# Kernel tuning notes

Measured on AMD Instinct MI355X. Metric: run time of the kernel, lower is better.

The kernel has to match this reference:

```python
import jax, jax.numpy as jnp
import numpy as np
from jax import lax

# --- Clifford algebra Cl(3,0): sig_g = [1,1,1], n_blades = 8 ---
SIG = np.array([1.0, 1.0, 1.0], dtype=np.float32)
N_GEN = len(SIG)
N_BLADES = 1 << N_GEN

def _build_cayley(g):
    # Structure constants C[a,b,c]: e_a * e_b = C[a,b,a^b] * e_{a^b}
    n = len(g); nb = 1 << n
    C = np.zeros((nb, nb, nb), dtype=np.float32)
    for a in range(nb):
        for b in range(nb):
            s = 1.0
            x = a >> 1
            while x:
                if bin(x & b).count('1') % 2:
                    s = -s
                x >>= 1
            common = a & b
            for k in range(n):
                if (common >> k) & 1:
                    s *= g[k]
            C[a, b, a ^ b] = s
    return C

CAYLEY = _build_cayley(SIG)
# blade signs: scalar coefficient of e_i * e_i (metric square of each blade)
BLADE_SIGNS = np.array([CAYLEY[i, i, 0] for i in range(N_BLADES)], dtype=np.float32)

DT = 0.1      # EPEngine dt
N_FREE = 5    # EPEngine n_free

def _energy(h, input_mv, W_rec, C, signs):
    # h: [B,L,H,I]
    rho = jnp.clip(h, 0.0, 1.0)
    E_self = 0.5 * jnp.sum(h * h, axis=(1, 2, 3))                       # [B]
    E_in = jnp.einsum('blhi,blhi,i->b', rho, input_mv, signs)           # [B]
    # causal recurrent term: geometric product of h_{l-1} with W_rec
    rec = jnp.einsum('blhi,ghj,ijk->blgk', rho[:, :-1], W_rec, C)       # [B,L-1,H,I]
    E_rec = jnp.einsum('blhk,blhk,k->b', rho[:, 1:], rec, signs)        # [B]
    return E_self - E_in - E_rec

def _free_phase(h0, input_mv, W_rec, C, signs):
    gfn = jax.grad(lambda h: jnp.sum(_energy(h, input_mv, W_rec, C, signs)))
    def step(h, _):
        return h - DT * gfn(h), None
    h, _ = lax.scan(step, h0, None, length=N_FREE)
    return h

def setup_inputs() -> dict:
    key = jax.random.key(0)
    ks = jax.random.split(key, 5)
    B, L, V, E, H = 4, 256, 32000, 256, 256
    x = jax.random.randint(ks[0], (B, L), 0, V)
    emb_table = jax.random.normal(ks[1], (V, E), jnp.float32)
    W_in = jax.random.normal(ks[2], (H, E, N_BLADES), jnp.float32) * 0.1
    W_rec = jax.random.normal(ks[3], (H, H, N_BLADES), jnp.float32) * 0.05
    W_out = jax.random.normal(ks[4], (V, H, N_BLADES), jnp.float32) * 0.1
    return {"x": x, "emb_table": emb_table, "W_in": W_in, "W_rec": W_rec, "W_out": W_out}

def reference(x, emb_table, W_in, W_rec, W_out):
    C = jnp.asarray(CAYLEY)
    signs = jnp.asarray(BLADE_SIGNS)
    emb = emb_table[x]                                  # [B,L,E]
    input_mv = jnp.einsum('bld,hdi->blhi', emb, W_in)   # [B,L,H,I]
    B, L = x.shape
    H = W_in.shape[0]
    h0 = jnp.zeros((B, L, H, N_BLADES), jnp.float32)
    h_free = _free_phase(h0, input_mv, W_rec, C, signs) # [B,L,H,I]
    # scalar part of geometric product of h_free with W_out (only blade 0 kept)
    logits = jnp.einsum('blhi,vhj,ij->blv', h_free, W_out, C[:, :, 0])
    return logits
```

## Files before the change

kernel.cpp:

```cpp
#include <hip/hip_runtime.h>
#include <cstddef>
#include <cstdint>

#define VOCAB  32000
#define EMB    256
#define NB     8
#define KDIM   2048
#define NROWS  1024
#define NCOL   4096
#define LLEN   256

typedef __attribute__((ext_vector_type(8))) short short8;
typedef __attribute__((ext_vector_type(4))) float f32x4;
typedef __attribute__((ext_vector_type(16))) float f32x16;
typedef __attribute__((ext_vector_type(4))) int i32x4;
typedef __attribute__((ext_vector_type(16))) int i32x16;

__device__ __forceinline__ float cl3_sign(int a, int b) {
  int x = a >> 1, p = 0;
  while (x) { p ^= __popc(x & b) & 1; x >>= 1; }
  return p ? -1.f : 1.f;
}

__device__ __forceinline__ float clipf(float v) { return fminf(fmaxf(v, 0.f), 1.f); }

__device__ __forceinline__ unsigned short f2bf(float f) {
  unsigned u = __float_as_uint(f);
  u += 0x7FFF + ((u >> 16) & 1);
  return (unsigned short)(u >> 16);
}
__device__ __forceinline__ float bf2f(unsigned short h) {
  return __uint_as_float(((unsigned)h) << 16);
}

__device__ __forceinline__ void gload16(const void* g, void* l) {
  __builtin_amdgcn_global_load_lds((const __attribute__((address_space(1))) uint32_t*)g,
                                   (__attribute__((address_space(3))) uint32_t*)l, 16, 0, 0);
}

__device__ __forceinline__ float dig_inv(float mx) {
  return exp2f((float)(5 - ilogbf(fmaxf(mx, 1e-20f))));
}

__device__ __forceinline__ size_t bfoff(int rt, int k, int r) {
  return ((size_t)(rt * 128 + (k >> 4)) << 11) + (size_t)(((k >> 3) & 1) << 10) + ((r & 127) << 3) + (k & 7);
}

__global__ void k_build_mrt_split(const float* __restrict__ Wrec,
                                  unsigned short* __restrict__ Mhi,
                                  unsigned short* __restrict__ Mlo) {
  int idx = blockIdx.x * blockDim.x + threadIdx.x;
  int k = idx & (KDIM - 1);
  int n = idx >> 11;
  int h = k >> 3, i = k & 7;
  float v;
  if (n < KDIM) {
    int g = n >> 3, kb = n & 7;
    int j = i ^ kb;
    v = Wrec[(size_t)g * KDIM + h * NB + j] * cl3_sign(i, j);
  } else {
    int c = n - KDIM;
    int p = c >> 3, q = c & 7;
    int j = q ^ i;
    v = cl3_sign(i, i) * cl3_sign(q, j) * Wrec[(size_t)h * KDIM + p * NB + j];
  }
  unsigned short hi = f2bf(v);
  unsigned short lo = f2bf(v - bf2f(hi));
  size_t off = bfoff(n >> 7, k, n);
  Mhi[off] = hi; Mlo[off] = lo;
}

__global__ __launch_bounds__(256) void k_dig_wout(const float* __restrict__ W,
                                                  float* __restrict__ sB,
                                                  char* __restrict__ Wd1,
                                                  char* __restrict__ Wd2) {
  __shared__ float ld[4 * 2052];
  __shared__ float rmax[4];
  const int t = threadIdx.x;
  const int bid = blockIdx.x;
  const float* src = W + (size_t)bid * 8192;
#pragma unroll
  for (int i = 0; i < 8; ++i) {
    int f = i * 256 + t;
    int row = f >> 9, c4 = f & 511;
    float4 v = ((const float4*)src)[f];
    *(float4*)&ld[row * 2052 + c4 * 4] = v;
  }
  __syncthreads();
  const int w = t >> 6, l = t & 63;
  float m = 0.f;
#pragma unroll
  for (int j = 0; j < 8; ++j) {
    float4 v = *(const float4*)&ld[w * 2052 + (j * 64 + l) * 4];
    m = fmaxf(m, fmaxf(fmaxf(fabsf(v.x), fabsf(v.y)), fmaxf(fabsf(v.z), fabsf(v.w))));
  }
#pragma unroll
  for (int s = 1; s < 64; s <<= 1) m = fmaxf(m, __shfl_xor(m, s));
  m = fmaxf(m, 1e-20f);
  if (l == 0) { rmax[w] = m; sB[bid * 4 + w] = exp2f((float)(ilogbf(m) + 2)); }
  __syncthreads();
  const int rloc = t & 3;
  const int rowg = bid * 4 + rloc;
  const int rowtile = rowg >> 7, rowin = rowg & 127;
  const float inv = dig_inv(rmax[rloc]);
#pragma unroll
  for (int it = 0; it < 2; ++it) {
    int c16 = (t >> 2) + it * 64;
    char d1[16], d2[16];
#pragma unroll
    for (int j = 0; j < 16; ++j) {
      float tv = ld[rloc * 2052 + c16 * 16 + j] * inv;
      float f1 = rintf(tv);
      d1[j] = (char)(int)f1;
      d2[j] = (char)(int)rintf((tv - f1) * 128.f);
    }
    size_t addr = ((size_t)(rowtile * 64 + (c16 >> 1)) << 12) + (size_t)((c16 & 1) << 11) + (rowin << 4);
    *(i32x4*)&Wd1[addr] = *(i32x4*)d1;
    *(i32x4*)&Wd2[addr] = *(i32x4*)d2;
  }
}

__global__ __launch_bounds__(256) void k_input_mv(const int* __restrict__ x,
                                                  const float* __restrict__ emb,
                                                  const float* __restrict__ Win,
                                                  float* __restrict__ out) {
  __shared__ float se[4][EMB];
  int r0 = blockIdx.x * 4;
  int t = threadIdx.x;
  for (int rr = 0; rr < 4; ++rr) {
    int tok = x[r0 + rr];
    se[rr][t] = emb[(size_t)tok * EMB + t];
  }
  __syncthreads();
  float acc[4][8];
#pragma unroll
  for (int rr = 0; rr < 4; ++rr)
#pragma unroll
    for (int i = 0; i < 8; ++i) acc[rr][i] = 0.f;
  const float* wrow = Win + (size_t)t * KDIM;
  for (int d = 0; d < EMB; ++d) {
    float4 w0 = *(const float4*)(wrow + d * 8);
    float4 w1 = *(const float4*)(wrow + d * 8 + 4);
#pragma unroll
    for (int rr = 0; rr < 4; ++rr) {
      float e = se[rr][d];
      acc[rr][0] += e * w0.x; acc[rr][1] += e * w0.y;
      acc[rr][2] += e * w0.z; acc[rr][3] += e * w0.w;
      acc[rr][4] += e * w1.x; acc[rr][5] += e * w1.y;
      acc[rr][6] += e * w1.z; acc[rr][7] += e * w1.w;
    }
  }
  for (int rr = 0; rr < 4; ++rr) {
    float4* o = (float4*)(out + (size_t)(r0 + rr) * KDIM + t * 8);
    o[0] = make_float4(acc[rr][0], acc[rr][1], acc[rr][2], acc[rr][3]);
    o[1] = make_float4(acc[rr][4], acc[rr][5], acc[rr][6], acc[rr][7]);
  }
}

__global__ __launch_bounds__(256, 2) void k_gemm_pre(const unsigned short* __restrict__ Ahi,
                                                     const unsigned short* __restrict__ Alo,
                                                     const unsigned short* __restrict__ Bhi,
                                                     const unsigned short* __restrict__ Blo,
                                                     float* __restrict__ RF0,
                                                     float* __restrict__ RF1) {
  __shared__ __align__(16) char lds[3 * 16384];
  const int b = blockIdx.x;
  const int lin = (b & 7) * 64 + (b >> 3);
  const int half = lin >> 8;
  const int rest = lin & 255;
  const int tm = rest & 7, tn = rest >> 3;
  const int ktbase = half * 64;
  float* __restrict__ C = half ? RF1 : RF0;
  const int t = threadIdx.x;
  const int l = t & 63, w = t >> 6;
  const int wr = w >> 1, wc = w & 1;

  const char* aHg = (const char*)Ahi + (((size_t)tm * 128 + ktbase) << 12) + (t << 4);
  const char* aLg = (const char*)Alo + (((size_t)tm * 128 + ktbase) << 12) + (t << 4);
  const char* bHg = (const char*)Bhi + (((size_t)tn * 128 + ktbase) << 12) + (t << 4);
  const char* bLg = (const char*)Blo + (((size_t)tn * 128 + ktbase) << 12) + (t << 4);
  const int wo = w << 10;

  f32x16 acc[2][2];
#pragma unroll
  for (int i = 0; i < 2; ++i)
#pragma unroll
    for (int j = 0; j < 2; ++j) acc[i][j] = (f32x16)0.f;

  auto STAGE = [&](int bf, int kt) {
    char* lb = &lds[bf * 16384];
    size_t kb = (size_t)kt << 12;
    gload16(aHg + kb, lb + wo);
    gload16(aLg + kb, lb + 4096 + wo);
    gload16(bHg + kb, lb + 8192 + wo);
    gload16(bLg + kb, lb + 12288 + wo);
  };

  STAGE(0, 0); STAGE(1, 1);

  const int ra = wr * 64 + (l & 31);
  const int rb = wc * 64 + (l & 31);
  const int cho = (l >> 5) << 11;
  int cur = 0;
  for (int kt = 0; kt < 64; ++kt) {
    int pf = cur + 2; if (pf >= 3) pf -= 3;
    if (kt < 63) { asm volatile("s_waitcnt vmcnt(4)" ::: "memory"); }
    else         { asm volatile("s_waitcnt vmcnt(0)" ::: "memory"); }
    __builtin_amdgcn_s_barrier();
    const char* lb = &lds[cur * 16384];
    short8 ah[2], al[2], bh[2], bl[2];
#pragma unroll
    for (int mi = 0; mi < 2; ++mi) {
      int off = cho + ((ra + mi * 32) << 4);
      ah[mi] = *(const short8*)(lb + off);
      al[mi] = *(const short8*)(lb + 4096 + off);
    }
#pragma unroll
    for (int nj = 0; nj < 2; ++nj) {
      int off = cho + ((rb + nj * 32) << 4);
      bh[nj] = *(const short8*)(lb + 8192 + off);
      bl[nj] = *(const short8*)(lb + 12288 + off);
    }
    if (kt + 2 < 64) STAGE(pf, kt + 2);
    __builtin_amdgcn_s_setprio(1);
#pragma unroll
    for (int mi = 0; mi < 2; ++mi)
#pragma unroll
      for (int nj = 0; nj < 2; ++nj) {
        acc[mi][nj] = __builtin_amdgcn_mfma_f32_32x32x16_bf16(ah[mi], bh[nj], acc[mi][nj], 0, 0, 0);
        acc[mi][nj] = __builtin_amdgcn_mfma_f32_32x32x16_bf16(ah[mi], bl[nj], acc[mi][nj], 0, 0, 0);
        acc[mi][nj] = __builtin_amdgcn_mfma_f32_32x32x16_bf16(al[mi], bh[nj], acc[mi][nj], 0, 0, 0);
      }
    __builtin_amdgcn_s_setprio(0);
    cur = (cur == 2) ? 0 : cur + 1;
  }

  const int rg0 = tm * 128 + wr * 64 + ((l >> 5) << 2);
  const int cg0 = tn * 128 + wc * 64 + (l & 31);
#pragma unroll
  for (int mi = 0; mi < 2; ++mi)
#pragma unroll
    for (int nj = 0; nj < 2; ++nj) {
      f32x16 v = acc[mi][nj];
#pragma unroll
      for (int g = 0; g < 16; ++g) {
        int rr = (g & 3) + ((g >> 2) << 3);
        C[(size_t)(rg0 + mi * 32 + rr) * NCOL + cg0 + nj * 32] = v[g];
      }
    }
}

__global__ __launch_bounds__(256, 2) void k_gemm_i8(const char* __restrict__ Ad1,
                                                    const char* __restrict__ Ad2,
                                                    const char* __restrict__ Bd1,
                                                    const char* __restrict__ Bd2,
                                                    const float* __restrict__ sA,
                                                    const float* __restrict__ sB,
                                                    float* __restrict__ C) {
  __shared__ __align__(16) char lds[3 * 16384];
  const int b = blockIdx.x;
  const int lin = (b & 7) * 250 + (b >> 3);
  const int tm = lin & 7, tn = lin >> 3;
  const int t = threadIdx.x;
  const int l = t & 63, w = t >> 6;
  const int wr = w >> 1, wc = w & 1;

  const char* a1g = Ad1 + (((size_t)tm * 64) << 12) + (t << 4);
  const char* a2g = Ad2 + (((size_t)tm * 64) << 12) + (t << 4);
  const char* b1g = Bd1 + (((size_t)tn * 64) << 12) + (t << 4);
  const char* b2g = Bd2 + (((size_t)tn * 64) << 12) + (t << 4);
  const int wo = w << 10;

  i32x16 acc1[2][2], acc2[2][2];
#pragma unroll
  for (int i = 0; i < 2; ++i)
#pragma unroll
    for (int j = 0; j < 2; ++j) { acc1[i][j] = (i32x16)0; acc2[i][j] = (i32x16)0; }

  auto STAGE = [&](int bf, int kt) {
    char* lb = &lds[bf * 16384];
    size_t kb = (size_t)kt << 12;
    gload16(a1g + kb, lb + wo);
    gload16(a2g + kb, lb + 4096 + wo);
    gload16(b1g + kb, lb + 8192 + wo);
    gload16(b2g + kb, lb + 12288 + wo);
  };

  STAGE(0, 0); STAGE(1, 1);

  const int ra = wr * 64 + (l & 31);
  const int rb = wc * 64 + (l & 31);
  const int kqo = (l >> 5) << 11;
  int cur = 0;
  for (int kt = 0; kt < 64; ++kt) {
    int pf = cur + 2; if (pf >= 3) pf -= 3;
    if (kt < 63) { asm volatile("s_waitcnt vmcnt(4)" ::: "memory"); }
    else         { asm volatile("s_waitcnt vmcnt(0)" ::: "memory"); }
    __builtin_amdgcn_s_barrier();
    const char* lb = &lds[cur * 16384];
    i32x4 a1[2], a2[2], b1[2], b2[2];
#pragma unroll
    for (int mi = 0; mi < 2; ++mi) {
      int off = kqo + ((ra + mi * 32) << 4);
      a1[mi] = *(const i32x4*)(lb + off);
      a2[mi] = *(const i32x4*)(lb + 4096 + off);
    }
#pragma unroll
    for (int nj = 0; nj < 2; ++nj) {
      int off = kqo + ((rb + nj * 32) << 4);
      b1[nj] = *(const i32x4*)(lb + 8192 + off);
      b2[nj] = *(const i32x4*)(lb + 12288 + off);
    }
    if (kt + 2 < 64) STAGE(pf, kt + 2);
    __builtin_amdgcn_s_setprio(1);
#pragma unroll
    for (int mi = 0; mi < 2; ++mi)
#pragma unroll
      for (int nj = 0; nj < 2; ++nj) {
        acc1[mi][nj] = __builtin_amdgcn_mfma_i32_32x32x32_i8(a1[mi], b1[nj], acc1[mi][nj], 0, 0, 0);
        acc2[mi][nj] = __builtin_amdgcn_mfma_i32_32x32x32_i8(a1[mi], b2[nj], acc2[mi][nj], 0, 0, 0);
        acc2[mi][nj] = __builtin_amdgcn_mfma_i32_32x32x32_i8(a2[mi], b1[nj], acc2[mi][nj], 0, 0, 0);
      }
    __builtin_amdgcn_s_setprio(0);
    cur = (cur == 2) ? 0 : cur + 1;
  }

  const int rbase = tm * 128 + wr * 64 + ((l >> 5) << 2);
  const int cb = tn * 128 + wc * 64 + (l & 31);
#pragma unroll
  for (int mi = 0; mi < 2; ++mi)
#pragma unroll
    for (int nj = 0; nj < 2; ++nj) {
      float sBv = sB[cb + nj * 32] * (1.f / 16384.f);
#pragma unroll
      for (int g = 0; g < 16; ++g) {
        int rr = (g & 3) + ((g >> 2) << 3);
        int row = rbase + mi * 32 + rr;
        float c1 = sA[row] * sBv;
        C[(size_t)row * VOCAB + cb + nj * 32] =
            fmaf((float)acc2[mi][nj][g], c1 * (1.f / 128.f), (float)acc1[mi][nj][g] * c1);
      }
    }
}

template <int LAST, int FIRST>
__global__ __launch_bounds__(256) void k_update(float* __restrict__ Hb, const float* __restrict__ Imv,
                                                const float* __restrict__ RF0, const float* __restrict__ RF1,
                                                unsigned short* __restrict__ Hhi,
                                                unsigned short* __restrict__ Hlo,
                                                float* __restrict__ sA,
                                                char* __restrict__ Ad1,
                                                char* __restrict__ Ad2,
                                                int big) {
  __shared__ float red[256];
  int tix = threadIdx.x;
  int idx = blockIdx.x * 256 + tix;
  int r = idx >> 8;
  int c = (idx & 255) << 3;
  int m = r & (LLEN - 1);
  const size_t base = (size_t)r * KDIM + c;
  float h[8], f[8];
  *(float4*)&h[0] = *(const float4*)(Hb + base);
  *(float4*)&h[4] = *(const float4*)(Hb + base + 4);
  float4 i0 = *(const float4*)(Imv + base);
  float4 i1 = *(const float4*)(Imv + base + 4);
  f[0] = i0.x; f[1] = i0.y; f[2] = i0.z; f[3] = i0.w;
  f[4] = i1.x; f[5] = i1.y; f[6] = i1.z; f[7] = i1.w;
#pragma unroll
  for (int j = 0; j < 8; ++j) f[j] *= ((0xE8 >> j) & 1) ? -1.f : 1.f;
  if (!FIRST) {
    if (m >= 1) {
      const float* rp0 = RF0 + (size_t)(r - 1) * NCOL + c;
      const float* rp1 = RF1 + (size_t)(r - 1) * NCOL + c;
#pragma unroll
      for (int j = 0; j < 8; ++j)
        f[j] += (rp0[j] + rp1[j]) * (((0xE8 >> j) & 1) ? -1.f : 1.f);
    }
    if (m < LLEN - 1) {
      const float* rn0 = RF0 + (size_t)(r + 1) * NCOL + KDIM + c;
      const float* rn1 = RF1 + (size_t)(r + 1) * NCOL + KDIM + c;
#pragma unroll
      for (int j = 0; j < 8; ++j) f[j] += rn0[j] + rn1[j];
    }
  }
  float hn[8], av[8];
#pragma unroll
  for (int j = 0; j < 8; ++j) {
    float hv = h[j];
    float dr = (hv > 0.f && hv < 1.f) ? 1.f : ((hv == 0.f || hv == 1.f) ? 0.5f : 0.f);
    hn[j] = hv - 0.1f * (hv - dr * f[j]);
  }
  *(float4*)(Hb + base) = make_float4(hn[0], hn[1], hn[2], hn[3]);
  *(float4*)(Hb + base + 4) = make_float4(hn[4], hn[5], hn[6], hn[7]);
  if (!LAST) {
    short8 h8, l8;
#pragma unroll
    for (int j = 0; j < 8; ++j) {
      float a = clipf(hn[j]);
      unsigned short hi = f2bf(a);
      h8[j] = (short)hi;
      l8[j] = (short)f2bf(a - bf2f(hi));
    }
    size_t off = bfoff(r >> 7, c, r);
    *(short8*)&Hhi[off] = h8;
    *(short8*)&Hlo[off] = l8;
  } else {
    if (!big) return;
#pragma unroll
    for (int j = 0; j < 8; ++j) av[j] = hn[j] * (((0xE8 >> j) & 1) ? -1.f : 1.f);
    float lm = 0.f;
#pragma unroll
    for (int j = 0; j < 8; ++j) lm = fmaxf(lm, fabsf(av[j]));
    red[tix] = lm; __syncthreads();
    for (int s = 128; s; s >>= 1) { if (tix < s) red[tix] = fmaxf(red[tix], red[tix + s]); __syncthreads(); }
    float mx = fmaxf(red[0], 1e-20f);
    float inv = dig_inv(mx);
    if (tix == 0) sA[r] = exp2f((float)(ilogbf(mx) + 2));
    char d1[8], d2[8];
#pragma unroll
    for (int j = 0; j < 8; ++j) {
      float tv = av[j] * inv;
      float f1 = rintf(tv);
      d1[j] = (char)(int)f1;
      d2[j] = (char)(int)rintf((tv - f1) * 128.f);
    }
    size_t addr = ((size_t)((r >> 7) * 64 + (c >> 5)) << 12) + (size_t)(((c >> 4) & 1) << 11)
                + ((r & 127) << 4) + (c & 15);
    *(uint64_t*)&Ad1[addr] = *(uint64_t*)d1;
    *(uint64_t*)&Ad2[addr] = *(uint64_t*)d2;
  }
}

template <int AMODE>
__global__ __launch_bounds__(256) void k_gemm_split(const float* __restrict__ A,
                                                    const float* __restrict__ B,
                                                    float* __restrict__ C, int ldc) {
  __shared__ unsigned short Ah[128 * 32], Al[128 * 32];
  __shared__ unsigned short Bh[128 * 32], Bl[128 * 32];
  const int t = threadIdx.x;
  const int row0 = blockIdx.y * 128, col0 = blockIdx.x * 128;
  const int l = t & 63, w = t >> 6;
  const int wr = w >> 1, wc = w & 1;
  const int sr = t >> 3;
  const int cc = (t & 7) << 2;
  const int chunkb = cc >> 3;
  const int halfo = (cc >> 2) & 1;
  f32x4 acc[4][4];
#pragma unroll
  for (int i = 0; i < 4; ++i)
#pragma unroll
    for (int j = 0; j < 4; ++j) acc[i][j] = (f32x4)0.f;
  const float sA0 = 1.f;
  const float sA1 = (cc & 4) ? -1.f : 1.f;
  const float sA2 = sA1;
  const float sA3 = -1.f;
  for (int k0 = 0; k0 < KDIM; k0 += 32) {
    float4 va[4], vb[4];
#pragma unroll
    for (int i = 0; i < 4; ++i) {
      va[i] = *(const float4*)(A + (size_t)(row0 + sr + i * 32) * KDIM + k0 + cc);
      vb[i] = *(const float4*)(B + (size_t)(col0 + sr + i * 32) * KDIM + k0 + cc);
    }
    __syncthreads();
#pragma unroll
    for (int i = 0; i < 4; ++i) {
      int row = sr + i * 32;
      int idx = row * 32 + ((chunkb ^ (row & 3)) << 3) + (halfo << 2);
      float4 a = va[i];
      if (AMODE == 0) {
        a.x = clipf(a.x); a.y = clipf(a.y); a.z = clipf(a.z); a.w = clipf(a.w);
      } else {
        a.x *= sA0; a.y *= sA1; a.z *= sA2; a.w *= sA3;
      }
      ushort4 h4, l4;
      h4.x = f2bf(a.x); l4.x = f2bf(a.x - bf2f(h4.x));
      h4.y = f2bf(a.y); l4.y = f2bf(a.y - bf2f(h4.y));
      h4.z = f2bf(a.z); l4.z = f2bf(a.z - bf2f(h4.z));
      h4.w = f2bf(a.w); l4.w = f2bf(a.w - bf2f(h4.w));
      *(ushort4*)&Ah[idx] = h4;
      *(ushort4*)&Al[idx] = l4;
      float4 bb = vb[i];
      h4.x = f2bf(bb.x); l4.x = f2bf(bb.x - bf2f(h4.x));
      h4.y = f2bf(bb.y); l4.y = f2bf(bb.y - bf2f(h4.y));
      h4.z = f2bf(bb.z); l4.z = f2bf(bb.z - bf2f(h4.z));
      h4.w = f2bf(bb.w); l4.w = f2bf(bb.w - bf2f(h4.w));
      *(ushort4*)&Bh[idx] = h4;
      *(ushort4*)&Bl[idx] = l4;
    }
    __syncthreads();
    short8 ah[4], al[4], bh[4], bl[4];
#pragma unroll
    for (int mi = 0; mi < 4; ++mi) {
      int ar = wr * 64 + mi * 16 + (l & 15);
      int kc = (l >> 4) ^ (ar & 3);
      ah[mi] = *(short8*)&Ah[ar * 32 + kc * 8];
      al[mi] = *(short8*)&Al[ar * 32 + kc * 8];
      int br = wc * 64 + mi * 16 + (l & 15);
      int kb = (l >> 4) ^ (br & 3);
      bh[mi] = *(short8*)&Bh[br * 32 + kb * 8];
      bl[mi] = *(short8*)&Bl[br * 32 + kb * 8];
    }
#pragma unroll
    for (int mi = 0; mi < 4; ++mi)
#pragma unroll
      for (int ni = 0; ni < 4; ++ni) {
        acc[mi][ni] = __builtin_amdgcn_mfma_f32_16x16x32_bf16(ah[mi], bh[ni], acc[mi][ni], 0, 0, 0);
        acc[mi][ni] = __builtin_amdgcn_mfma_f32_16x16x32_bf16(ah[mi], bl[ni], acc[mi][ni], 0, 0, 0);
        acc[mi][ni] = __builtin_amdgcn_mfma_f32_16x16x32_bf16(al[mi], bh[ni], acc[mi][ni], 0, 0, 0);
      }
  }
#pragma unroll
  for (int mi = 0; mi < 4; ++mi)
#pragma unroll
    for (int ni = 0; ni < 4; ++ni) {
      int rg = row0 + wr * 64 + mi * 16 + (l >> 4) * 4;
      int cg = col0 + wc * 64 + ni * 16 + (l & 15);
#pragma unroll
      for (int j = 0; j < 4; ++j)
        C[(size_t)(rg + j) * ldc + cg] = acc[mi][ni][j];
    }
}

extern "C" void kernel_launch(void* const* d_in, const int* in_sizes, int n_in,
                              void* d_out, int out_size, void* d_ws, size_t ws_size,
                              hipStream_t stream) {
  const int*   x    = (const int*)d_in[0];
  const float* emb  = (const float*)d_in[1];
  const float* Win  = (const float*)d_in[2];
  const float* Wrec = (const float*)d_in[3];
  const float* Wout = (const float*)d_in[4];
  float* logits = (float*)d_out;

  char* base = (char*)d_ws;
  const size_t MB = 1ull << 20;
  float* Hbuf = (float*)(base + 0);
  float* Imv  = (float*)(base + 8 * MB);
  float* RF0  = (float*)(base + 16 * MB);
  float* RF1  = (float*)(base + 32 * MB);
  unsigned short* Hhi = (unsigned short*)(base + 48 * MB);
  unsigned short* Hlo = (unsigned short*)(base + 52 * MB);
  unsigned short* Mhi = (unsigned short*)(base + 56 * MB);
  unsigned short* Mlo = (unsigned short*)(base + 72 * MB);
  float* sA  = (float*)(base + 88 * MB);
  float* sB  = (float*)(base + 88 * MB + 4096);
  char* Wd1  = base + 88 * MB + 160 * 1024;
  char* Wd2  = Wd1 + (size_t)VOCAB * KDIM;
  char* Ad1  = (char*)Mhi;
  char* Ad2  = (char*)Mlo;

  const size_t need = (size_t)(Wd2 - base) + (size_t)VOCAB * KDIM;
  const bool big = ws_size >= need;

  hipMemsetAsync(Hbuf, 0, 8 * MB, stream);
  k_build_mrt_split<<<32768, 256, 0, stream>>>(Wrec, Mhi, Mlo);
  k_input_mv<<<256, 256, 0, stream>>>(x, emb, Win, Imv);
  if (big) {
    k_dig_wout<<<8000, 256, 0, stream>>>(Wout, sB, Wd1, Wd2);
  }

  k_update<0, 1><<<1024, 256, 0, stream>>>(Hbuf, Imv, RF0, RF1, Hhi, Hlo, sA, Ad1, Ad2, big);
  for (int it = 1; it < 5; ++it) {
    k_gemm_pre<<<512, 256, 0, stream>>>(Hhi, Hlo, Mhi, Mlo, RF0, RF1);
    if (it < 4) k_update<0, 0><<<1024, 256, 0, stream>>>(Hbuf, Imv, RF0, RF1, Hhi, Hlo, sA, Ad1, Ad2, big);
    else        k_update<1, 0><<<1024, 256, 0, stream>>>(Hbuf, Imv, RF0, RF1, Hhi, Hlo, sA, Ad1, Ad2, big);
  }

  if (big) {
    k_gemm_i8<<<2000, 256, 0, stream>>>(Ad1, Ad2, Wd1, Wd2, sA, sB, logits);
  } else {
    k_gemm_split<1><<<dim3(VOCAB / 128, NROWS / 128), 256, 0, stream>>>(Hbuf, Wout, logits, VOCAB);
  }
}
```

Before: 631.2 us.

## Halve GEMM N-tile to 64 with higher occupancy and fuse first update into input_mv

```diff
diff --git a/kernel.cpp b/kernel.cpp
--- a/kernel.cpp
+++ b/kernel.cpp
@@ -120,10 +120,13 @@
   }
 }
 
-__global__ __launch_bounds__(256) void k_input_mv(const int* __restrict__ x,
+__global__ __launch_bounds__(256) void k_input_h1(const int* __restrict__ x,
                                                   const float* __restrict__ emb,
                                                   const float* __restrict__ Win,
-                                                  float* __restrict__ out) {
+                                                  float* __restrict__ Imv,
+                                                  float* __restrict__ Hb,
+                                                  unsigned short* __restrict__ Hhi,
+                                                  unsigned short* __restrict__ Hlo) {
   __shared__ float se[4][EMB];
   int r0 = blockIdx.x * 4;
   int t = threadIdx.x;
@@ -150,200 +153,208 @@
       acc[rr][6] += e * w1.z; acc[rr][7] += e * w1.w;
     }
   }
+  const int c = t * 8;
   for (int rr = 0; rr < 4; ++rr) {
-    float4* o = (float4*)(out + (size_t)(r0 + rr) * KDIM + t * 8);
-    o[0] = make_float4(acc[rr][0], acc[rr][1], acc[rr][2], acc[rr][3]);
-    o[1] = make_float4(acc[rr][4], acc[rr][5], acc[rr][6], acc[rr][7]);
-  }
-}
-
-__global__ __launch_bounds__(256, 2) void k_gemm_pre(const unsigned short* __restrict__ Ahi,
+    int r = r0 + rr;
+    float* o = Imv + (size_t)r * KDIM + c;
+    *(float4*)o = make_float4(acc[rr][0], acc[rr][1], acc[rr][2], acc[rr][3]);
+    *(float4*)(o + 4) = make_float4(acc[rr][4], acc[rr][5], acc[rr][6], acc[rr][7]);
+    float hn[8];
+    short8 h8, l8;
+#pragma unroll
+    for (int j = 0; j < 8; ++j) {
+      float f = acc[rr][j] * (((0xE8 >> j) & 1) ? -1.f : 1.f);
+      hn[j] = 0.f - 0.1f * (0.f - 0.5f * f);
+      float a = clipf(hn[j]);
+      unsigned short hi = f2bf(a);
+      h8[j] = (short)hi;
+      l8[j] = (short)f2bf(a - bf2f(hi));
+    }
+    float* hb = Hb + (size_t)r * KDIM + c;
+    *(float4*)hb = make_float4(hn[0], hn[1], hn[2], hn[3]);
+    *(float4*)(hb + 4) = make_float4(hn[4], hn[5], hn[6], hn[7]);
+    size_t off = bfoff(r >> 7, c, r);
+    *(short8*)&Hhi[off] = h8;
+    *(short8*)&Hlo[off] = l8;
+  }
+}
+
+__global__ __launch_bounds__(256, 4) void k_gemm_pre(const unsigned short* __restrict__ Ahi,
                                                      const unsigned short* __restrict__ Alo,
                                                      const unsigned short* __restrict__ Bhi,
                                                      const unsigned short* __restrict__ Blo,
                                                      float* __restrict__ RF0,
                                                      float* __restrict__ RF1) {
-  __shared__ __align__(16) char lds[3 * 16384];
+  __shared__ __align__(16) char lds[3 * 12288];
   const int b = blockIdx.x;
-  const int lin = (b & 7) * 64 + (b >> 3);
-  const int half = lin >> 8;
-  const int rest = lin & 255;
-  const int tm = rest & 7, tn = rest >> 3;
+  const int lin = (b & 7) * 128 + (b >> 3);
+  const int tm = lin & 7;
+  const int rest = lin >> 3;
+  const int tn = rest & 63, half = rest >> 6;
   const int ktbase = half * 64;
   float* __restrict__ C = half ? RF1 : RF0;
   const int t = threadIdx.x;
   const int l = t & 63, w = t >> 6;
   const int wr = w >> 1, wc = w & 1;
-
-  const char* aHg = (const char*)Ahi + (((size_t)tm * 128 + ktbase) << 12) + (t << 4);
-  const char* aLg = (const char*)Alo + (((size_t)tm * 128 + ktbase) << 12) + (t << 4);
-  const char* bHg = (const char*)Bhi + (((size_t)tn * 128 + ktbase) << 12) + (t << 4);
-  const char* bLg = (const char*)Blo + (((size_t)tn * 128 + ktbase) << 12) + (t << 4);
   const int wo = w << 10;
 
-  f32x16 acc[2][2];
-#pragma unroll
-  for (int i = 0; i < 2; ++i)
-#pragma unroll
-    for (int j = 0; j < 2; ++j) acc[i][j] = (f32x16)0.f;
+  const char* aHg = (const char*)Ahi + (((size_t)(tm * 128 + ktbase)) << 12) + (t << 4);
+  const char* aLg = (const char*)Alo + (((size_t)(tm * 128 + ktbase)) << 12) + (t << 4);
+  const int jj = t & 127;
+  const int bt = tn >> 1, r0b = (tn & 1) << 6;
+  const char* bGg = (const char*)((t >> 7) ? Blo : Bhi)
+                  + (((size_t)(bt * 128 + ktbase)) << 12)
+                  + ((jj >> 6) << 11) + ((size_t)(r0b + (jj & 63)) << 4);
+
+  f32x16 acc[2];
+  acc[0] = (f32x16)0.f; acc[1] = (f32x16)0.f;
 
   auto STAGE = [&](int bf, int kt) {
-    char* lb = &lds[bf * 16384];
+    char* lb = &lds[bf * 12288];
     size_t kb = (size_t)kt << 12;
     gload16(aHg + kb, lb + wo);
     gload16(aLg + kb, lb + 4096 + wo);
-    gload16(bHg + kb, lb + 8192 + wo);
-    gload16(bLg + kb, lb + 12288 + wo);
+    gload16(bGg + kb, lb + 8192 + wo);
   };
 
   STAGE(0, 0); STAGE(1, 1);
 
   const int ra = wr * 64 + (l & 31);
-  const int rb = wc * 64 + (l & 31);
-  const int cho = (l >> 5) << 11;
+  const int rb = wc * 32 + (l & 31);
+  const int kq = l >> 5;
   int cur = 0;
   for (int kt = 0; kt < 64; ++kt) {
     int pf = cur + 2; if (pf >= 3) pf -= 3;
-    if (kt < 63) { asm volatile("s_waitcnt vmcnt(4)" ::: "memory"); }
+    if (kt < 63) { asm volatile("s_waitcnt vmcnt(3)" ::: "memory"); }
     else         { asm volatile("s_waitcnt vmcnt(0)" ::: "memory"); }
     __builtin_amdgcn_s_barrier();
-    const char* lb = &lds[cur * 16384];
-    short8 ah[2], al[2], bh[2], bl[2];
+    const char* lb = &lds[cur * 12288];
+    short8 ah[2], al[2], bh, bl;
 #pragma unroll
     for (int mi = 0; mi < 2; ++mi) {
-      int off = cho + ((ra + mi * 32) << 4);
+      int off = (kq << 11) + ((ra + mi * 32) << 4);
       ah[mi] = *(const short8*)(lb + off);
       al[mi] = *(const short8*)(lb + 4096 + off);
     }
-#pragma unroll
-    for (int nj = 0; nj < 2; ++nj) {
-      int off = cho + ((rb + nj * 32) << 4);
-      bh[nj] = *(const short8*)(lb + 8192 + off);
-      bl[nj] = *(const short8*)(lb + 12288 + off);
+    {
+      int off = (kq << 10) + (rb << 4);
+      bh = *(const short8*)(lb + 8192 + off);
+      bl = *(const short8*)(lb + 10240 + off);
     }
     if (kt + 2 < 64) STAGE(pf, kt + 2);
     __builtin_amdgcn_s_setprio(1);
 #pragma unroll
-    for (int mi = 0; mi < 2; ++mi)
-#pragma unroll
-      for (int nj = 0; nj < 2; ++nj) {
-        acc[mi][nj] = __builtin_amdgcn_mfma_f32_32x32x16_bf16(ah[mi], bh[nj], acc[mi][nj], 0, 0, 0);
-        acc[mi][nj] = __builtin_amdgcn_mfma_f32_32x32x16_bf16(ah[mi], bl[nj], acc[mi][nj], 0, 0, 0);
-        acc[mi][nj] = __builtin_amdgcn_mfma_f32_32x32x16_bf16(al[mi], bh[nj], acc[mi][nj], 0, 0, 0);
-      }
+    for (int mi = 0; mi < 2; ++mi) {
+      acc[mi] = __builtin_amdgcn_mfma_f32_32x32x16_bf16(ah[mi], bh, acc[mi], 0, 0, 0);
+      acc[mi] = __builtin_amdgcn_mfma_f32_32x32x16_bf16(ah[mi], bl, acc[mi], 0, 0, 0);
+      acc[mi] = __builtin_amdgcn_mfma_f32_32x32x16_bf16(al[mi], bh, acc[mi], 0, 0, 0);
+    }
     __builtin_amdgcn_s_setprio(0);
     cur = (cur == 2) ? 0 : cur + 1;
   }
 
   const int rg0 = tm * 128 + wr * 64 + ((l >> 5) << 2);
-  const int cg0 = tn * 128 + wc * 64 + (l & 31);
-#pragma unroll
-  for (int mi = 0; mi < 2; ++mi)
-#pragma unroll
-    for (int nj = 0; nj < 2; ++nj) {
-      f32x16 v = acc[mi][nj];
-#pragma unroll
-      for (int g = 0; g < 16; ++g) {
-        int rr = (g & 3) + ((g >> 2) << 3);
-        C[(size_t)(rg0 + mi * 32 + rr) * NCOL + cg0 + nj * 32] = v[g];
-      }
-    }
-}
-
-__global__ __launch_bounds__(256, 2) void k_gemm_i8(const char* __restrict__ Ad1,
+  const int cg0 = tn * 64 + wc * 32 + (l & 31);
+#pragma unroll
+  for (int mi = 0; mi < 2; ++mi) {
+    f32x16 v = acc[mi];
+#pragma unroll
+    for (int g = 0; g < 16; ++g) {
+      int rr = (g & 3) + ((g >> 2) << 3);
+      C[(size_t)(rg0 + mi * 32 + rr) * NCOL + cg0] = v[g];
+    }
+  }
+}
+
+__global__ __launch_bounds__(256, 3) void k_gemm_i8(const char* __restrict__ Ad1,
                                                     const char* __restrict__ Ad2,
                                                     const char* __restrict__ Bd1,
                                                     const char* __restrict__ Bd2,
                                                     const float* __restrict__ sA,
                                                     const float* __restrict__ sB,
                                                     float* __restrict__ C) {
-  __shared__ __align__(16) char lds[3 * 16384];
+  __shared__ __align__(16) char lds[3 * 12288];
   const int b = blockIdx.x;
-  const int lin = (b & 7) * 250 + (b >> 3);
+  const int lin = (b & 7) * 500 + (b >> 3);
   const int tm = lin & 7, tn = lin >> 3;
   const int t = threadIdx.x;
   const int l = t & 63, w = t >> 6;
   const int wr = w >> 1, wc = w & 1;
+  const int wo = w << 10;
 
   const char* a1g = Ad1 + (((size_t)tm * 64) << 12) + (t << 4);
   const char* a2g = Ad2 + (((size_t)tm * 64) << 12) + (t << 4);
-  const char* b1g = Bd1 + (((size_t)tn * 64) << 12) + (t << 4);
-  const char* b2g = Bd2 + (((size_t)tn * 64) << 12) + (t << 4);
-  const int wo = w << 10;
-
-  i32x16 acc1[2][2], acc2[2][2];
-#pragma unroll
-  for (int i = 0; i < 2; ++i)
-#pragma unroll
-    for (int j = 0; j < 2; ++j) { acc1[i][j] = (i32x16)0; acc2[i][j] = (i32x16)0; }
+  const int jj = t & 127;
+  const int wt = tn >> 1, r0b = (tn & 1) << 6;
+  const char* bGg = ((t >> 7) ? Bd2 : Bd1)
+                  + (((size_t)wt * 64) << 12)
+                  + ((jj >> 6) << 11) + ((size_t)(r0b + (jj & 63)) << 4);
+
+  i32x16 acc1[2], acc2[2];
+  acc1[0] = (i32x16)0; acc1[1] = (i32x16)0;
+  acc2[0] = (i32x16)0; acc2[1] = (i32x16)0;
 
   auto STAGE = [&](int bf, int kt) {
-    char* lb = &lds[bf * 16384];
+    char* lb = &lds[bf * 12288];
     size_t kb = (size_t)kt << 12;
     gload16(a1g + kb, lb + wo);
     gload16(a2g + kb, lb + 4096 + wo);
-    gload16(b1g + kb, lb + 8192 + wo);
-    gload16(b2g + kb, lb + 12288 + wo);
+    gload16(bGg + kb, lb + 8192 + wo);
   };
 
   STAGE(0, 0); STAGE(1, 1);
 
   const int ra = wr * 64 + (l & 31);
-  const int rb = wc * 64 + (l & 31);
-  const int kqo = (l >> 5) << 11;
+  const int rb = wc * 32 + (l & 31);
+  const int kq = l >> 5;
   int cur = 0;
   for (int kt = 0; kt < 64; ++kt) {
     int pf = cur + 2; if (pf >= 3) pf -= 3;
-    if (kt < 63) { asm volatile("s_waitcnt vmcnt(4)" ::: "memory"); }
+    if (kt < 63) { asm volatile("s_waitcnt vmcnt(3)" ::: "memory"); }
     else         { asm volatile("s_waitcnt vmcnt(0)" ::: "memory"); }
     __builtin_amdgcn_s_barrier();
-    const char* lb = &lds[cur * 16384];
-    i32x4 a1[2], a2[2], b1[2], b2[2];
+    const char* lb = &lds[cur * 12288];
+    i32x4 a1[2], a2[2], b1, b2;
 #pragma unroll
     for (int mi = 0; mi < 2; ++mi) {
-      int off = kqo + ((ra + mi * 32) << 4);
+      int off = (kq << 11) + ((ra + mi * 32) << 4);
       a1[mi] = *(const i32x4*)(lb + off);
       a2[mi] = *(const i32x4*)(lb + 4096 + off);
     }
-#pragma unroll
-    for (int nj = 0; nj < 2; ++nj) {
-      int off = kqo + ((rb + nj * 32) << 4);
-      b1[nj] = *(const i32x4*)(lb + 8192 + off);
-      b2[nj] = *(const i32x4*)(lb + 12288 + off);
+    {
+      int off = (kq << 10) + (rb << 4);
+      b1 = *(const i32x4*)(lb + 8192 + off);
+      b2 = *(const i32x4*)(lb + 10240 + off);
     }
     if (kt + 2 < 64) STAGE(pf, kt + 2);
     __builtin_amdgcn_s_setprio(1);
 #pragma unroll
-    for (int mi = 0; mi < 2; ++mi)
-#pragma unroll
-      for (int nj = 0; nj < 2; ++nj) {
-        acc1[mi][nj] = __builtin_amdgcn_mfma_i32_32x32x32_i8(a1[mi], b1[nj], acc1[mi][nj], 0, 0, 0);
-        acc2[mi][nj] = __builtin_amdgcn_mfma_i32_32x32x32_i8(a1[mi], b2[nj], acc2[mi][nj], 0, 0, 0);
-        acc2[mi][nj] = __builtin_amdgcn_mfma_i32_32x32x32_i8(a2[mi], b1[nj], acc2[mi][nj], 0, 0, 0);
-      }
+    for (int mi = 0; mi < 2; ++mi) {
+      acc1[mi] = __builtin_amdgcn_mfma_i32_32x32x32_i8(a1[mi], b1, acc1[mi], 0, 0, 0);
+      acc2[mi] = __builtin_amdgcn_mfma_i32_32x32x32_i8(a1[mi], b2, acc2[mi], 0, 0, 0);
+      acc2[mi] = __builtin_amdgcn_mfma_i32_32x32x32_i8(a2[mi], b1, acc2[mi], 0, 0, 0);
+    }
     __builtin_amdgcn_s_setprio(0);
     cur = (cur == 2) ? 0 : cur + 1;
   }
 
   const int rbase = tm * 128 + wr * 64 + ((l >> 5) << 2);
-  const int cb = tn * 128 + wc * 64 + (l & 31);
-#pragma unroll
-  for (int mi = 0; mi < 2; ++mi)
-#pragma unroll
-    for (int nj = 0; nj < 2; ++nj) {
-      float sBv = sB[cb + nj * 32] * (1.f / 16384.f);
-#pragma unroll
-      for (int g = 0; g < 16; ++g) {
-        int rr = (g & 3) + ((g >> 2) << 3);
-        int row = rbase + mi * 32 + rr;
-        float c1 = sA[row] * sBv;
-        C[(size_t)row * VOCAB + cb + nj * 32] =
-            fmaf((float)acc2[mi][nj][g], c1 * (1.f / 128.f), (float)acc1[mi][nj][g] * c1);
-      }
-    }
-}
-
-template <int LAST, int FIRST>
+  const int cb = tn * 64 + wc * 32 + (l & 31);
+  const float sBv = sB[cb] * (1.f / 16384.f);
+#pragma unroll
+  for (int mi = 0; mi < 2; ++mi) {
+#pragma unroll
+    for (int g = 0; g < 16; ++g) {
+      int rr = (g & 3) + ((g >> 2) << 3);
+      int row = rbase + mi * 32 + rr;
+      float c1 = sA[row] * sBv;
+      C[(size_t)row * VOCAB + cb] =
+          fmaf((float)acc2[mi][g], c1 * (1.f / 128.f), (float)acc1[mi][g] * c1);
+    }
+  }
+}
+
+template <int LAST>
 __global__ __launch_bounds__(256) void k_update(float* __restrict__ Hb, const float* __restrict__ Imv,
                                                 const float* __restrict__ RF0, const float* __restrict__ RF1,
                                                 unsigned short* __restrict__ Hhi,
@@ -368,20 +379,18 @@
   f[4] = i1.x; f[5] = i1.y; f[6] = i1.z; f[7] = i1.w;
 #pragma unroll
   for (int j = 0; j < 8; ++j) f[j] *= ((0xE8 >> j) & 1) ? -1.f : 1.f;
-  if (!FIRST) {
-    if (m >= 1) {
-      const float* rp0 = RF0 + (size_t)(r - 1) * NCOL + c;
-      const float* rp1 = RF1 + (size_t)(r - 1) * NCOL + c;
-#pragma unroll
-      for (int j = 0; j < 8; ++j)
-        f[j] += (rp0[j] + rp1[j]) * (((0xE8 >> j) & 1) ? -1.f : 1.f);
-    }
-    if (m < LLEN - 1) {
-      const float* rn0 = RF0 + (size_t)(r + 1) * NCOL + KDIM + c;
-      const float* rn1 = RF1 + (size_t)(r + 1) * NCOL + KDIM + c;
-#pragma unroll
-      for (int j = 0; j < 8; ++j) f[j] += rn0[j] + rn1[j];
-    }
+  if (m >= 1) {
+    const float* rp0 = RF0 + (size_t)(r - 1) * NCOL + c;
+    const float* rp1 = RF1 + (size_t)(r - 1) * NCOL + c;
+#pragma unroll
+    for (int j = 0; j < 8; ++j)
+      f[j] += (rp0[j] + rp1[j]) * (((0xE8 >> j) & 1) ? -1.f : 1.f);
+  }
+  if (m < LLEN - 1) {
+    const float* rn0 = RF0 + (size_t)(r + 1) * NCOL + KDIM + c;
+    const float* rn1 = RF1 + (size_t)(r + 1) * NCOL + KDIM + c;
+#pragma unroll
+    for (int j = 0; j < 8; ++j) f[j] += rn0[j] + rn1[j];
   }
   float hn[8], av[8];
 #pragma unroll
@@ -551,22 +560,20 @@
   const size_t need = (size_t)(Wd2 - base) + (size_t)VOCAB * KDIM;
   const bool big = ws_size >= need;
 
-  hipMemsetAsync(Hbuf, 0, 8 * MB, stream);
   k_build_mrt_split<<<32768, 256, 0, stream>>>(Wrec, Mhi, Mlo);
-  k_input_mv<<<256, 256, 0, stream>>>(x, emb, Win, Imv);
+  k_input_h1<<<256, 256, 0, stream>>>(x, emb, Win, Imv, Hbuf, Hhi, Hlo);
   if (big) {
     k_dig_wout<<<8000, 256, 0, stream>>>(Wout, sB, Wd1, Wd2);
   }
 
-  k_update<0, 1><<<1024, 256, 0, stream>>>(Hbuf, Imv, RF0, RF1, Hhi, Hlo, sA, Ad1, Ad2, big);
   for (int it = 1; it < 5; ++it) {
-    k_gemm_pre<<<512, 256, 0, stream>>>(Hhi, Hlo, Mhi, Mlo, RF0, RF1);
-    if (it < 4) k_update<0, 0><<<1024, 256, 0, stream>>>(Hbuf, Imv, RF0, RF1, Hhi, Hlo, sA, Ad1, Ad2, big);
-    else        k_update<1, 0><<<1024, 256, 0, stream>>>(Hbuf, Imv, RF0, RF1, Hhi, Hlo, sA, Ad1, Ad2, big);
+    k_gemm_pre<<<1024, 256, 0, stream>>>(Hhi, Hlo, Mhi, Mlo, RF0, RF1);
+    if (it < 4) k_update<0><<<1024, 256, 0, stream>>>(Hbuf, Imv, RF0, RF1, Hhi, Hlo, sA, Ad1, Ad2, big);
+    else        k_update<1><<<1024, 256, 0, stream>>>(Hbuf, Imv, RF0, RF1, Hhi, Hlo, sA, Ad1, Ad2, big);
   }
 
   if (big) {
-    k_gemm_i8<<<2000, 256, 0, stream>>>(Ad1, Ad2, Wd1, Wd2, sA, sB, logits);
+    k_gemm_i8<<<4000, 256, 0, stream>>>(Ad1, Ad2, Wd1, Wd2, sA, sB, logits);
   } else {
     k_gemm_split<1><<<dim3(VOCAB / 128, NROWS / 128), 256, 0, stream>>>(Hbuf, Wout, logits, VOCAB);
   }
```

Measured after the change: 694.9 us. +10.1%, slower.
